# Performance work log

Measured on AMD Instinct MI355X. Metric: run time of the kernel, lower is better.

## Reference

```python
import jax, jax.numpy as jnp
import numpy as np

K = 6  # hardcoded top-k in the original forward


def setup_inputs() -> dict:
    key = jax.random.key(0)
    k1, k2, k3, k4, k5 = jax.random.split(key, 5)
    N, M, C = 512, 2048, 256
    return {
        "micro": jax.random.normal(k1, (N, C), jnp.float32),
        "label": jax.random.uniform(k2, (N,), jnp.float32),
        "micro_all": jax.random.normal(k3, (M, C), jnp.float32),
        "label_all": jax.random.uniform(k4, (M,), jnp.float32),
        # fc = nn.Linear(channels, 1, bias=False) -> weight vector [C]
        "fc_w": jax.random.normal(k5, (C,), jnp.float32) * 0.05,
    }


def reference(micro, label, micro_all, label_all, fc_w):
    N, C = micro.shape
    M = micro_all.shape[0]
    # Pairwise squared differences: dis[n, m, c] = (micro_all[m,c] - micro[n,c])^2
    dis = (micro_all[None, :, :] - micro[:, None, :]) ** 2  # [N, M, C]
    # Linear(C,1,bias=False) along channel dim, minus per-pair channel mean
    anti = jnp.einsum('nmc,c->nm', dis, fc_w) - dis.mean(axis=2)  # [N, M]
    anti = jax.nn.softmax(anti, axis=1)
    # top-k mask (argsort-based selection of k largest == lax.top_k)
    _, idx = jax.lax.top_k(anti, K)  # [N, K]
    mask = jnp.zeros((N, M), anti.dtype).at[jnp.arange(N)[:, None], idx].set(1.0)
    cut = anti * mask
    cut = cut / jnp.sum(cut, axis=1, keepdims=True)  # renormalize kNN weights
    micro_tmp = micro + cut @ micro_all  # [N, C]
    # composition loss
    dis_label = jnp.abs(label_all[None, :] - label[:, None])  # [N, M]
    co_loss = jnp.asarray(1e-4, cut.dtype) + jnp.sum(dis_label * cut) / N
    return micro_tmp, co_loss
```

## Files before the change

### kernel.cpp

```cpp
#include <hip/hip_runtime.h>
#include <hip/hip_bf16.h>
#include <math.h>

#define N_Q   512
#define M_ALL 2048
#define CHN   256
#define TOPK  6
#define INV_C (1.0f / 256.0f)

#define WS_LOSS  64
#define WS_LOGIT 4096

#define BM 64
#define BN 32
#define KC 64
#define LDA (BM + 4)
#define LDB (BN + 4)

__global__ __launch_bounds__(256) void gcn_gemm(
    const float* __restrict__ micro_all,
    const float* __restrict__ micro,
    const float* __restrict__ fc_w,
    float* __restrict__ logits)
{
    __shared__ float As[KC][LDA];
    __shared__ float Bs[KC][LDB];
    __shared__ float s_w[CHN];
    __shared__ float s_bias[BM];

    const int t  = threadIdx.x;
    const int m0 = blockIdx.x * BM;
    const int n0 = blockIdx.y * BN;
    const int tm = t & 15;
    const int tn = t >> 4;

    s_w[t] = fc_w[t] - INV_C;
    __syncthreads();

    float acc00 = 0.f, acc01 = 0.f, acc10 = 0.f, acc11 = 0.f;
    float acc20 = 0.f, acc21 = 0.f, acc30 = 0.f, acc31 = 0.f;
    float biasAcc[4] = {0.f, 0.f, 0.f, 0.f};

    for (int kc0 = 0; kc0 < CHN; kc0 += KC) {
        #pragma unroll
        for (int i = 0; i < 4; ++i) {
            const int item = t + i * 256;
            const int r = item >> 4, c4 = item & 15;
            float4 v = *(const float4*)(micro_all + (size_t)(m0 + r) * CHN + kc0 + c4 * 4);
            const float sx = v.x * s_w[kc0 + c4 * 4 + 0];
            const float sy = v.y * s_w[kc0 + c4 * 4 + 1];
            const float sz = v.z * s_w[kc0 + c4 * 4 + 2];
            const float sw = v.w * s_w[kc0 + c4 * 4 + 3];
            As[c4 * 4 + 0][r] = sx;
            As[c4 * 4 + 1][r] = sy;
            As[c4 * 4 + 2][r] = sz;
            As[c4 * 4 + 3][r] = sw;
            float p = v.x * sx + v.y * sy + v.z * sz + v.w * sw;
            #pragma unroll
            for (int mask = 8; mask >= 1; mask >>= 1)
                p += __shfl_xor(p, mask, 16);
            biasAcc[i] += p;
        }
        #pragma unroll
        for (int i = 0; i < 2; ++i) {
            const int item = t + i * 256;
            const int r = item >> 4, c4 = item & 15;
            float4 v = *(const float4*)(micro + (size_t)(n0 + r) * CHN + kc0 + c4 * 4);
            Bs[c4 * 4 + 0][r] = v.x;
            Bs[c4 * 4 + 1][r] = v.y;
            Bs[c4 * 4 + 2][r] = v.z;
            Bs[c4 * 4 + 3][r] = v.w;
        }
        __syncthreads();

        #pragma unroll 16
        for (int k = 0; k < KC; ++k) {
            const float4 a = *(const float4*)&As[k][tm * 4];
            const float2 b = *(const float2*)&Bs[k][tn * 2];
            acc00 += a.x * b.x; acc01 += a.x * b.y;
            acc10 += a.y * b.x; acc11 += a.y * b.y;
            acc20 += a.z * b.x; acc21 += a.z * b.y;
            acc30 += a.w * b.x; acc31 += a.w * b.y;
        }
        __syncthreads();
    }

    if ((t & 15) == 0) {
        #pragma unroll
        for (int i = 0; i < 4; ++i)
            s_bias[i * 16 + (t >> 4)] = biasAcc[i];
    }
    __syncthreads();

    const float4 bi = *(const float4*)&s_bias[tm * 4];
    {
        const int n = n0 + tn * 2;
        float4 o;
        o.x = bi.x - 2.f * acc00;
        o.y = bi.y - 2.f * acc10;
        o.z = bi.z - 2.f * acc20;
        o.w = bi.w - 2.f * acc30;
        *(float4*)&logits[(size_t)n * M_ALL + m0 + tm * 4] = o;
    }
    {
        const int n = n0 + tn * 2 + 1;
        float4 o;
        o.x = bi.x - 2.f * acc01;
        o.y = bi.y - 2.f * acc11;
        o.z = bi.z - 2.f * acc21;
        o.w = bi.w - 2.f * acc31;
        *(float4*)&logits[(size_t)n * M_ALL + m0 + tm * 4] = o;
    }
}

#define BLOCK 256
#define WAVES (BLOCK / 64)
#define MPT   (M_ALL / BLOCK)
#define NCAND (WAVES * TOPK)

__global__ __launch_bounds__(BLOCK) void gcn_topk(
    const float* __restrict__ logits,
    const float* __restrict__ micro,
    const float* __restrict__ label,
    const float* __restrict__ micro_all,
    const float* __restrict__ label_all,
    float* __restrict__ out,
    float* __restrict__ loss_arr)
{
    __shared__ float s_cv[NCAND];
    __shared__ int   s_ci[NCAND];

    const int n    = blockIdx.x;
    const int t    = threadIdx.x;
    const int wave = t >> 6;
    const int lane = t & 63;

    float logit[MPT];
    #pragma unroll
    for (int j = 0; j < MPT; ++j)
        logit[j] = logits[(size_t)n * M_ALL + t + j * BLOCK];

    unsigned taken = 0u;
    float wv[TOPK];
    int   wi[TOPK];
    #pragma unroll
    for (int k = 0; k < TOPK; ++k) {
        float best  = -INFINITY;
        int   bestj = -1;
        #pragma unroll
        for (int j = 0; j < MPT; ++j) {
            bool avail = ((taken >> j) & 1u) == 0u;
            if (avail && logit[j] > best) { best = logit[j]; bestj = j; }
        }
        float v  = best;
        int   mi = (bestj < 0) ? -1 : (t + bestj * BLOCK);
        #pragma unroll
        for (int mask = 32; mask > 0; mask >>= 1) {
            float ov = __shfl_xor(v,  mask, 64);
            int   om = __shfl_xor(mi, mask, 64);
            if (ov > v) { v = ov; mi = om; }
        }
        wv[k] = v;
        wi[k] = mi;
        if (mi >= 0 && t == (mi & (BLOCK - 1))) taken |= 1u << (mi >> 8);
    }
    if (lane == 0) {
        #pragma unroll
        for (int k = 0; k < TOPK; ++k) {
            s_cv[wave * TOPK + k] = wv[k];
            s_ci[wave * TOPK + k] = wi[k];
        }
    }
    __syncthreads();

    float top_val[TOPK];
    int   top_idx[TOPK];
    unsigned ctk = 0u;
    #pragma unroll
    for (int k = 0; k < TOPK; ++k) {
        float best = -INFINITY;
        int   bi   = 0;
        #pragma unroll
        for (int c = 0; c < NCAND; ++c) {
            bool avail = ((ctk >> c) & 1u) == 0u;
            float cv = s_cv[c];
            if (avail && cv > best) { best = cv; bi = c; }
        }
        top_val[k] = best;
        top_idx[k] = s_ci[bi];
        ctk |= 1u << bi;
    }

    const float mx = top_val[0];
    float e[TOPK];
    float esum = 0.0f;
    #pragma unroll
    for (int k = 0; k < TOPK; ++k) { e[k] = __expf(top_val[k] - mx); esum += e[k]; }
    const float inv = 1.0f / esum;

    float outv = micro[(size_t)n * CHN + t];
    #pragma unroll
    for (int k = 0; k < TOPK; ++k)
        outv += (e[k] * inv) * micro_all[(size_t)top_idx[k] * CHN + t];
    out[n * CHN + t] = outv;

    if (t == 0) {
        const float lab = label[n];
        float l = 0.0f;
        #pragma unroll
        for (int k = 0; k < TOPK; ++k)
            l += (e[k] * inv) * fabsf(label_all[top_idx[k]] - lab);
        loss_arr[n] = l;
    }
}

__global__ __launch_bounds__(256) void gcn_finalize(
    const float* __restrict__ loss_arr,
    float* __restrict__ out)
{
    __shared__ float red[4];
    const int t = threadIdx.x;
    float v = loss_arr[t] + loss_arr[t + 256];
    #pragma unroll
    for (int mask = 32; mask >= 1; mask >>= 1)
        v += __shfl_xor(v, mask, 64);
    if ((t & 63) == 0) red[t >> 6] = v;
    __syncthreads();
    if (t == 0)
        out[N_Q * CHN] = 1e-4f + (red[0] + red[1] + red[2] + red[3]) / (float)N_Q;
}

extern "C" void kernel_launch(void* const* d_in, const int* in_sizes, int n_in,
                              void* d_out, int out_size, void* d_ws, size_t ws_size,
                              hipStream_t stream) {
    const float* micro     = (const float*)d_in[0];
    const float* label     = (const float*)d_in[1];
    const float* micro_all = (const float*)d_in[2];
    const float* label_all = (const float*)d_in[3];
    const float* fc_w      = (const float*)d_in[4];
    float* out    = (float*)d_out;
    float* ws     = (float*)d_ws;
    float* loss   = ws + WS_LOSS;
    float* logits = ws + WS_LOGIT;

    gcn_gemm<<<dim3(M_ALL / BM, N_Q / BN), 256, 0, stream>>>(
        micro_all, micro, fc_w, logits);
    gcn_topk<<<N_Q, BLOCK, 0, stream>>>(logits, micro, label, micro_all,
                                        label_all, out, loss);
    gcn_finalize<<<1, 256, 0, stream>>>(loss, out);
}
```

Baseline: 96.14 us.

## Use bf16 MFMA for logit GEMM with exact fp32 rescoring of top candidates

The logit GEMM now converts the weighted micro_all and micro tiles to bf16 in shared memory over the full channel depth and computes them with 16x16x32 bf16 MFMA instructions, replacing the scalar fp32 FMA loop. To make up for the lost precision, the top-k kernel takes 8 candidates per wave, keeps the best 10 overall, recomputes their exact fp32 weighted distances from the raw features, and picks the final 6 from those. This adds extra global reads and reductions per query. Selection could still differ from the reference if the true top-6 falls outside the bf16-ranked top-10.

```diff
diff --git a/kernel.cpp b/kernel.cpp
--- a/kernel.cpp
+++ b/kernel.cpp
@@ -11,11 +11,19 @@
 #define WS_LOSS  64
 #define WS_LOGIT 4096
 
+typedef __bf16 bf16x8 __attribute__((ext_vector_type(8)));
+typedef float  f32x4  __attribute__((ext_vector_type(4)));
+
+static __device__ __forceinline__ unsigned short bfbits(float x) {
+    __bf16 h = (__bf16)x;
+    unsigned short u;
+    __builtin_memcpy(&u, &h, 2);
+    return u;
+}
+
 #define BM 64
 #define BN 32
-#define KC 64
-#define LDA (BM + 4)
-#define LDB (BN + 4)
+#define LDK 264
 
 __global__ __launch_bounds__(256) void gcn_gemm(
     const float* __restrict__ micro_all,
@@ -23,100 +31,99 @@
     const float* __restrict__ fc_w,
     float* __restrict__ logits)
 {
-    __shared__ float As[KC][LDA];
-    __shared__ float Bs[KC][LDB];
-    __shared__ float s_w[CHN];
+    __shared__ unsigned short sA[BM][LDK];
+    __shared__ unsigned short sB[BN][LDK];
     __shared__ float s_bias[BM];
 
-    const int t  = threadIdx.x;
-    const int m0 = blockIdx.x * BM;
-    const int n0 = blockIdx.y * BN;
-    const int tm = t & 15;
-    const int tn = t >> 4;
-
-    s_w[t] = fc_w[t] - INV_C;
-    __syncthreads();
-
-    float acc00 = 0.f, acc01 = 0.f, acc10 = 0.f, acc11 = 0.f;
-    float acc20 = 0.f, acc21 = 0.f, acc30 = 0.f, acc31 = 0.f;
-    float biasAcc[4] = {0.f, 0.f, 0.f, 0.f};
-
-    for (int kc0 = 0; kc0 < CHN; kc0 += KC) {
-        #pragma unroll
-        for (int i = 0; i < 4; ++i) {
-            const int item = t + i * 256;
-            const int r = item >> 4, c4 = item & 15;
-            float4 v = *(const float4*)(micro_all + (size_t)(m0 + r) * CHN + kc0 + c4 * 4);
-            const float sx = v.x * s_w[kc0 + c4 * 4 + 0];
-            const float sy = v.y * s_w[kc0 + c4 * 4 + 1];
-            const float sz = v.z * s_w[kc0 + c4 * 4 + 2];
-            const float sw = v.w * s_w[kc0 + c4 * 4 + 3];
-            As[c4 * 4 + 0][r] = sx;
-            As[c4 * 4 + 1][r] = sy;
-            As[c4 * 4 + 2][r] = sz;
-            As[c4 * 4 + 3][r] = sw;
-            float p = v.x * sx + v.y * sy + v.z * sz + v.w * sw;
-            #pragma unroll
-            for (int mask = 8; mask >= 1; mask >>= 1)
-                p += __shfl_xor(p, mask, 16);
-            biasAcc[i] += p;
-        }
-        #pragma unroll
-        for (int i = 0; i < 2; ++i) {
-            const int item = t + i * 256;
-            const int r = item >> 4, c4 = item & 15;
-            float4 v = *(const float4*)(micro + (size_t)(n0 + r) * CHN + kc0 + c4 * 4);
-            Bs[c4 * 4 + 0][r] = v.x;
-            Bs[c4 * 4 + 1][r] = v.y;
-            Bs[c4 * 4 + 2][r] = v.z;
-            Bs[c4 * 4 + 3][r] = v.w;
-        }
-        __syncthreads();
-
-        #pragma unroll 16
-        for (int k = 0; k < KC; ++k) {
-            const float4 a = *(const float4*)&As[k][tm * 4];
-            const float2 b = *(const float2*)&Bs[k][tn * 2];
-            acc00 += a.x * b.x; acc01 += a.x * b.y;
-            acc10 += a.y * b.x; acc11 += a.y * b.y;
-            acc20 += a.z * b.x; acc21 += a.z * b.y;
-            acc30 += a.w * b.x; acc31 += a.w * b.y;
-        }
-        __syncthreads();
-    }
-
-    if ((t & 15) == 0) {
-        #pragma unroll
-        for (int i = 0; i < 4; ++i)
-            s_bias[i * 16 + (t >> 4)] = biasAcc[i];
-    }
-    __syncthreads();
-
-    const float4 bi = *(const float4*)&s_bias[tm * 4];
-    {
-        const int n = n0 + tn * 2;
-        float4 o;
-        o.x = bi.x - 2.f * acc00;
-        o.y = bi.y - 2.f * acc10;
-        o.z = bi.z - 2.f * acc20;
-        o.w = bi.w - 2.f * acc30;
-        *(float4*)&logits[(size_t)n * M_ALL + m0 + tm * 4] = o;
-    }
-    {
-        const int n = n0 + tn * 2 + 1;
-        float4 o;
-        o.x = bi.x - 2.f * acc01;
-        o.y = bi.y - 2.f * acc11;
-        o.z = bi.z - 2.f * acc21;
-        o.w = bi.w - 2.f * acc31;
-        *(float4*)&logits[(size_t)n * M_ALL + m0 + tm * 4] = o;
+    const int t    = threadIdx.x;
+    const int w    = t >> 6;
+    const int l15  = t & 15;
+    const int quad = (t >> 4) & 3;
+    const int m0   = blockIdx.x * BM;
+    const int n0   = blockIdx.y * BN;
+
+    const int rg = t >> 4;
+    const int c0 = (t & 15) * 4;
+
+    float4 wv[4];
+    #pragma unroll
+    for (int cc = 0; cc < 4; ++cc) {
+        float4 x = *(const float4*)(fc_w + c0 + cc * 64);
+        x.x -= INV_C; x.y -= INV_C; x.z -= INV_C; x.w -= INV_C;
+        wv[cc] = x;
+    }
+
+    #pragma unroll
+    for (int i = 0; i < 4; ++i) {
+        const int r = i * 16 + rg;
+        const float* rp = micro_all + (size_t)(m0 + r) * CHN;
+        float p = 0.0f;
+        #pragma unroll
+        for (int cc = 0; cc < 4; ++cc) {
+            const float4 v = *(const float4*)(rp + c0 + cc * 64);
+            const float sx = v.x * wv[cc].x;
+            const float sy = v.y * wv[cc].y;
+            const float sz = v.z * wv[cc].z;
+            const float sw = v.w * wv[cc].w;
+            ushort4 pk;
+            pk.x = bfbits(sx); pk.y = bfbits(sy); pk.z = bfbits(sz); pk.w = bfbits(sw);
+            *(ushort4*)&sA[r][c0 + cc * 64] = pk;
+            p += v.x * sx + v.y * sy + v.z * sz + v.w * sw;
+        }
+        #pragma unroll
+        for (int mask = 8; mask >= 1; mask >>= 1)
+            p += __shfl_xor(p, mask, 64);
+        if ((t & 15) == 0) s_bias[r] = p;
+    }
+
+    #pragma unroll
+    for (int i = 0; i < 2; ++i) {
+        const int r = i * 16 + rg;
+        const float* rp = micro + (size_t)(n0 + r) * CHN;
+        #pragma unroll
+        for (int cc = 0; cc < 4; ++cc) {
+            const float4 v = *(const float4*)(rp + c0 + cc * 64);
+            ushort4 pk;
+            pk.x = bfbits(v.x); pk.y = bfbits(v.y); pk.z = bfbits(v.z); pk.w = bfbits(v.w);
+            *(ushort4*)&sB[r][c0 + cc * 64] = pk;
+        }
+    }
+    __syncthreads();
+
+    const int nt    = w & 1;
+    const int mtp   = w >> 1;
+    const int rowB  = nt * 16 + l15;
+    const int rowA0 = mtp * 32 + l15;
+    const int rowA1 = mtp * 32 + 16 + l15;
+
+    f32x4 acc0 = {0.f, 0.f, 0.f, 0.f};
+    f32x4 acc1 = {0.f, 0.f, 0.f, 0.f};
+    #pragma unroll
+    for (int ks = 0; ks < 8; ++ks) {
+        const int k0 = ks * 32 + quad * 8;
+        const bf16x8 a  = *(const bf16x8*)&sB[rowB][k0];
+        const bf16x8 b0 = *(const bf16x8*)&sA[rowA0][k0];
+        const bf16x8 b1 = *(const bf16x8*)&sA[rowA1][k0];
+        acc0 = __builtin_amdgcn_mfma_f32_16x16x32_bf16(a, b0, acc0, 0, 0, 0);
+        acc1 = __builtin_amdgcn_mfma_f32_16x16x32_bf16(a, b1, acc1, 0, 0, 0);
+    }
+
+    const float bias0 = s_bias[mtp * 32 + l15];
+    const float bias1 = s_bias[mtp * 32 + 16 + l15];
+    #pragma unroll
+    for (int reg = 0; reg < 4; ++reg) {
+        const int n = n0 + nt * 16 + quad * 4 + reg;
+        logits[(size_t)n * M_ALL + m0 + mtp * 32 + l15]      = bias0 - 2.f * acc0[reg];
+        logits[(size_t)n * M_ALL + m0 + mtp * 32 + 16 + l15] = bias1 - 2.f * acc1[reg];
     }
 }
 
 #define BLOCK 256
 #define WAVES (BLOCK / 64)
 #define MPT   (M_ALL / BLOCK)
-#define NCAND (WAVES * TOPK)
+#define WTOP  8
+#define NCAND (WAVES * WTOP)
+#define NREF  10
 
 __global__ __launch_bounds__(BLOCK) void gcn_topk(
     const float* __restrict__ logits,
@@ -124,27 +131,31 @@
     const float* __restrict__ label,
     const float* __restrict__ micro_all,
     const float* __restrict__ label_all,
+    const float* __restrict__ fc_w,
     float* __restrict__ out,
     float* __restrict__ loss_arr)
 {
     __shared__ float s_cv[NCAND];
     __shared__ int   s_ci[NCAND];
+    __shared__ float s_ex[NREF];
 
     const int n    = blockIdx.x;
     const int t    = threadIdx.x;
     const int wave = t >> 6;
     const int lane = t & 63;
 
+    float4 b4 = *(const float4*)(micro + (size_t)n * CHN + lane * 4);
+    float4 w4 = *(const float4*)(fc_w + lane * 4);
+    w4.x -= INV_C; w4.y -= INV_C; w4.z -= INV_C; w4.w -= INV_C;
+
     float logit[MPT];
     #pragma unroll
     for (int j = 0; j < MPT; ++j)
         logit[j] = logits[(size_t)n * M_ALL + t + j * BLOCK];
 
     unsigned taken = 0u;
-    float wv[TOPK];
-    int   wi[TOPK];
-    #pragma unroll
-    for (int k = 0; k < TOPK; ++k) {
+    #pragma unroll
+    for (int k = 0; k < WTOP; ++k) {
         float best  = -INFINITY;
         int   bestj = -1;
         #pragma unroll
@@ -160,24 +171,19 @@
             int   om = __shfl_xor(mi, mask, 64);
             if (ov > v) { v = ov; mi = om; }
         }
-        wv[k] = v;
-        wi[k] = mi;
+        if (lane == 0) {
+            s_cv[wave * WTOP + k] = v;
+            s_ci[wave * WTOP + k] = mi;
+        }
         if (mi >= 0 && t == (mi & (BLOCK - 1))) taken |= 1u << (mi >> 8);
     }
-    if (lane == 0) {
-        #pragma unroll
-        for (int k = 0; k < TOPK; ++k) {
-            s_cv[wave * TOPK + k] = wv[k];
-            s_ci[wave * TOPK + k] = wi[k];
-        }
-    }
-    __syncthreads();
-
-    float top_val[TOPK];
-    int   top_idx[TOPK];
+    __syncthreads();
+
+    float tv[NREF];
+    int   ti[NREF];
     unsigned ctk = 0u;
     #pragma unroll
-    for (int k = 0; k < TOPK; ++k) {
+    for (int k = 0; k < NREF; ++k) {
         float best = -INFINITY;
         int   bi   = 0;
         #pragma unroll
@@ -186,9 +192,42 @@
             float cv = s_cv[c];
             if (avail && cv > best) { best = cv; bi = c; }
         }
+        tv[k] = best;
+        ti[k] = s_ci[bi];
+        ctk |= 1u << bi;
+    }
+
+    for (int c = wave; c < NREF; c += WAVES) {
+        const int m = ti[c];
+        const float4 a = *(const float4*)(micro_all + (size_t)m * CHN + lane * 4);
+        const float dx = a.x - b4.x;
+        const float dy = a.y - b4.y;
+        const float dz = a.z - b4.z;
+        const float dw = a.w - b4.w;
+        float acc = dx * dx * w4.x + dy * dy * w4.y + dz * dz * w4.z + dw * dw * w4.w;
+        #pragma unroll
+        for (int mask = 32; mask >= 1; mask >>= 1)
+            acc += __shfl_xor(acc, mask, 64);
+        if (lane == 0) s_ex[c] = acc;
+    }
+    __syncthreads();
+
+    float top_val[TOPK];
+    int   top_idx[TOPK];
+    unsigned rtk = 0u;
+    #pragma unroll
+    for (int k = 0; k < TOPK; ++k) {
+        float best = -INFINITY;
+        int   bi   = 0;
+        #pragma unroll
+        for (int c = 0; c < NREF; ++c) {
+            bool avail = ((rtk >> c) & 1u) == 0u;
+            float cv = s_ex[c];
+            if (avail && cv > best) { best = cv; bi = c; }
+        }
         top_val[k] = best;
-        top_idx[k] = s_ci[bi];
-        ctk |= 1u << bi;
+        top_idx[k] = ti[bi];
+        rtk |= 1u << bi;
     }
 
     const float mx = top_val[0];
@@ -246,6 +285,6 @@
     gcn_gemm<<<dim3(M_ALL / BM, N_Q / BN), 256, 0, stream>>>(
         micro_all, micro, fc_w, logits);
     gcn_topk<<<N_Q, BLOCK, 0, stream>>>(logits, micro, label, micro_all,
-                                        label_all, out, loss);
+                                        label_all, fc_w, out, loss);
     gcn_finalize<<<1, 256, 0, stream>>>(loss, out);
 }
```

Measured after the change: 87.45 us. 9.0% less time.
